# Optimization experiments

Measured on AMD Instinct MI355X. Metric: run time of the kernel, lower is better.

## Reference

```python
import jax, jax.numpy as jnp
import numpy as np

ALPHA = 0.2  # LeakyReLU negative slope
NEG = -9e15


def _gat_heads(x, adj_mask, W, a):
    # x: (B,N,F); W: (H,F,O); a: (H,2O); adj_mask: (B,N,N) bool
    O = W.shape[-1]
    Wh = jnp.einsum('bnf,hfo->bhno', x, W)            # (B,H,N,O)
    e1 = jnp.einsum('bhno,ho->bhn', Wh, a[:, :O])     # Wh @ a[:O]
    e2 = jnp.einsum('bhno,ho->bhn', Wh, a[:, O:])     # Wh @ a[O:]
    e = jax.nn.leaky_relu(e1[:, :, :, None] + e2[:, :, None, :], ALPHA)  # (B,H,N,N)
    e = jnp.where(adj_mask[:, None], e, NEG)
    attn = jax.nn.softmax(e, axis=-1)
    return jnp.einsum('bhnm,bhmo->bhno', attn, Wh)    # (B,H,N,O)


def _gat_block(x, adj_mask, non_pad_mask, W_heads, a_heads, W_out, a_out):
    # multi-head layer, concat=True -> elu per head, then concat on feature dim
    h = jax.nn.elu(_gat_heads(x, adj_mask, W_heads, a_heads))  # (B,H,N,O)
    B, H, N, O = h.shape
    h = jnp.transpose(h, (0, 2, 1, 3)).reshape(B, N, H * O)
    h = h * non_pad_mask
    # out layer: single head, concat=False (no inner elu)
    h = _gat_heads(h, adj_mask, W_out[None], a_out[None])[:, 0]  # (B,N,noutput)
    h = h * non_pad_mask
    return jax.nn.elu(h)


def setup_inputs() -> dict:
    key = jax.random.key(0)
    ks = jax.random.split(key, 8)
    B, N = 32, 256
    vocab, F, O, H, OUT = 200, 300, 256, 8, 512
    fea = jax.random.randint(ks[0], (B, N), 0, vocab, dtype=jnp.int32)
    adj = jax.random.randint(ks[1], (B, N, N), 0, 2, dtype=jnp.int32)
    non_pad_mask = jnp.ones((B, N, 1), dtype=jnp.float32)
    embed = jax.random.normal(ks[2], (vocab, F), dtype=jnp.float32)
    W_heads = jax.random.normal(ks[3], (H, F, O), dtype=jnp.float32) / np.sqrt(F)
    a_heads = jax.random.normal(ks[4], (H, 2 * O), dtype=jnp.float32) / np.sqrt(2 * O)
    W_out = jax.random.normal(ks[5], (H * O, OUT), dtype=jnp.float32) / np.sqrt(H * O)
    a_out = jax.random.normal(ks[6], (2 * OUT,), dtype=jnp.float32) / np.sqrt(2 * OUT)
    return {"fea": fea, "adj": adj, "non_pad_mask": non_pad_mask, "embed": embed,
            "W_heads": W_heads, "a_heads": a_heads, "W_out": W_out, "a_out": a_out}


def reference(fea, adj, non_pad_mask, embed, W_heads, a_heads, W_out, a_out):
    adj_mask = adj > 0
    x = embed[fea]  # (B,N,F)
    # GAT_num = 1; dropout is identity in eval mode
    x = _gat_block(x, adj_mask, non_pad_mask, W_heads, a_heads, W_out, a_out)
    return x  # (B, N, 512)
```

## Files before the change

kernel.cpp:

```cpp
#include <hip/hip_runtime.h>
#include <math.h>


typedef _Float16 f16;
typedef __attribute__((ext_vector_type(8))) _Float16 f16x8;
typedef __attribute__((ext_vector_type(4))) _Float16 f16x4;
typedef __attribute__((ext_vector_type(4))) float f32x4;

__device__ __forceinline__ void async16(const void* g, void* lds) {
  __builtin_amdgcn_global_load_lds(
      (const __attribute__((address_space(1))) void*)g,
      (__attribute__((address_space(3))) void*)lds, 16, 0, 0);
}

__global__ __launch_bounds__(256) void k_prep(const int* __restrict__ fea,
                                              const float* __restrict__ embed,
                                              const float* __restrict__ Whd,
                                              const float* __restrict__ Wo,
                                              f16* __restrict__ x16,
                                              f16* __restrict__ WcT,
                                              f16* __restrict__ WoT,
                                              float* __restrict__ e_all) {
  int bid = blockIdx.x, tid = threadIdx.x;
  if (bid < 1280) {
    int idx = bid * 256 + tid;
    int row = idx / 40, c = idx % 40;
    int tok = fea[row];
    const float* eb = embed + (size_t)tok * 300;
    f16x8 v;
#pragma unroll
    for (int j = 0; j < 8; ++j) {
      int t = c * 8 + j;
      v[j] = (f16)((t < 300) ? eb[t] : 0.f);
    }
    *(f16x8*)&x16[(size_t)row * 320 + c * 8] = v;
  } else if (bid < 1920) {
    int r = bid - 1280;
    int zi = r * 256 + tid;
    if (zi < 147456) e_all[zi] = 0.f;
    __shared__ float tile[32][33];
    int bx = r % 10, q0 = r / 10;
    int by = q0 % 8, h = q0 / 8;
    int c = tid & 31, q = tid >> 5;
#pragma unroll
    for (int i = 0; i < 4; ++i) {
      int tt = q + i * 8;
      int t = bx * 32 + tt;
      float v = (t < 300) ? Whd[((size_t)h * 300 + t) * 256 + by * 32 + c] : 0.f;
      tile[tt][c] = v;
    }
    __syncthreads();
#pragma unroll
    for (int i = 0; i < 4; ++i) {
      int oo = q + i * 8;
      int gc = h * 256 + by * 32 + oo;
      WcT[(size_t)gc * 320 + bx * 32 + c] = (f16)tile[c][oo];
    }
  } else {
    int r = bid - 1920;
    __shared__ float tile[32][33];
    int bx = r % 64, by = r / 64;
    int c = tid & 31, q = tid >> 5;
#pragma unroll
    for (int i = 0; i < 4; ++i) {
      int kk = q + i * 8;
      tile[kk][c] = Wo[((size_t)bx * 32 + kk) * 512 + by * 32 + c];
    }
    __syncthreads();
#pragma unroll
    for (int i = 0; i < 4; ++i) {
      int oo = q + i * 8;
      WoT[((size_t)by * 32 + oo) * 2048 + bx * 32 + c] = (f16)tile[c][oo];
    }
  }
}

template <int KDIM, int NCOLS>
__global__ __launch_bounds__(256, 4) void k_gemm1(const f16* __restrict__ A,
                                                  const f16* __restrict__ BT,
                                                  f16* __restrict__ outT,
                                                  const float* __restrict__ avec,
                                                  float* __restrict__ e1,
                                                  float* __restrict__ e2) {
  __shared__ f16 As[128 * 64];
  __shared__ f16 Bs[128 * 64];
  const int by = blockIdx.x, bx = blockIdx.y;
  const int tid = threadIdx.x;
  const int wave = tid >> 6, lane = tid & 63;
  const int wm = wave >> 1, wn = wave & 1;
  const int lrow = lane & 15, quad = lane >> 4;
  const int srow = lane >> 3;
  const int scol = ((lane & 7) ^ (lane >> 3)) * 8;
  const int l7 = lrow & 7;

  f32x4 acc[4][4] = {};
  const f16* Ag = A + (size_t)by * 128 * KDIM;
  const f16* Bg = BT + (size_t)bx * 128 * KDIM;

  for (int k0 = 0; k0 < KDIM; k0 += 64) {
    __syncthreads();
#pragma unroll
    for (int j = 0; j < 4; ++j) {
      const int r0 = wave * 32 + j * 8;
      async16(Ag + (size_t)(r0 + srow) * KDIM + k0 + scol, &As[r0 * 64]);
      async16(Bg + (size_t)(r0 + srow) * KDIM + k0 + scol, &Bs[r0 * 64]);
    }
    __syncthreads();
#pragma unroll
    for (int s = 0; s < 2; ++s) {
      const int sq = ((s * 4 + quad) ^ l7) * 8;
      f16x8 af[4], bf[4];
#pragma unroll
      for (int t = 0; t < 4; ++t) {
        af[t] = *(const f16x8*)&As[(wm * 64 + t * 16 + lrow) * 64 + sq];
        bf[t] = *(const f16x8*)&Bs[(wn * 64 + t * 16 + lrow) * 64 + sq];
      }
#pragma unroll
      for (int mt = 0; mt < 4; ++mt)
#pragma unroll
        for (int nt = 0; nt < 4; ++nt)
          acc[mt][nt] = __builtin_amdgcn_mfma_f32_16x16x32_f16(af[mt], bf[nt], acc[mt][nt], 0, 0, 0);
    }
  }

  const int b = (by * 128) >> 8;
  const int nbase0 = (by * 128) & 255;
#pragma unroll
  for (int mt = 0; mt < 4; ++mt) {
    const int nb = nbase0 + wm * 64 + mt * 16 + quad * 4;
#pragma unroll
    for (int nt = 0; nt < 4; ++nt) {
      const int gc = bx * 128 + wn * 64 + nt * 16 + lrow;
      f16x4 v;
#pragma unroll
      for (int r = 0; r < 4; ++r) v[r] = (f16)acc[mt][nt][r];
      *(f16x4*)&outT[((size_t)b * NCOLS + gc) * 256 + nb] = v;
    }
  }

  float a1v[4], a2v[4];
#pragma unroll
  for (int nt = 0; nt < 4; ++nt) {
    const int gc = bx * 128 + wn * 64 + nt * 16 + lrow;
    int hh = gc >> 8, oo = gc & 255;
    a1v[nt] = avec[hh * 512 + oo];
    a2v[nt] = avec[hh * 512 + 256 + oo];
  }
  const int hblk = (bx * 128) >> 8;
  const int ebase = (b * 8 + hblk) * 256;
#pragma unroll
  for (int mt = 0; mt < 4; ++mt) {
    float s1[4] = {0.f, 0.f, 0.f, 0.f}, s2[4] = {0.f, 0.f, 0.f, 0.f};
#pragma unroll
    for (int nt = 0; nt < 4; ++nt)
#pragma unroll
      for (int r = 0; r < 4; ++r) {
        s1[r] += acc[mt][nt][r] * a1v[nt];
        s2[r] += acc[mt][nt][r] * a2v[nt];
      }
#pragma unroll
    for (int r = 0; r < 4; ++r)
#pragma unroll
      for (int m = 1; m < 16; m <<= 1) {
        s1[r] += __shfl_xor(s1[r], m);
        s2[r] += __shfl_xor(s2[r], m);
      }
    if (lrow == 0) {
      const int nb = nbase0 + wm * 64 + mt * 16 + quad * 4;
#pragma unroll
      for (int r = 0; r < 4; ++r) {
        atomicAdd(&e1[ebase + nb + r], s1[r]);
        atomicAdd(&e2[ebase + nb + r], s2[r]);
      }
    }
  }
}

__global__ __launch_bounds__(256, 4) void k_gemm_sk(const f16* __restrict__ A,
                                                    const f16* __restrict__ BT,
                                                    f16* __restrict__ outSK) {
  __shared__ f16 As[128 * 64];
  __shared__ f16 Bs[64 * 64];
  const int by = blockIdx.x, bx = blockIdx.y, kz = blockIdx.z;
  const int tid = threadIdx.x;
  const int wave = tid >> 6, lane = tid & 63;
  const int wm = wave >> 1, wn = wave & 1;
  const int lrow = lane & 15, quad = lane >> 4;
  const int srow = lane >> 3;
  const int scol = ((lane & 7) ^ (lane >> 3)) * 8;
  const int l7 = lrow & 7;

  f32x4 acc[4][2] = {};
  const f16* Ag = A + (size_t)by * 128 * 2048;
  const f16* Bg = BT + (size_t)bx * 64 * 2048;
  const int kbeg = kz * 1024;

  for (int k0 = kbeg; k0 < kbeg + 1024; k0 += 64) {
    __syncthreads();
#pragma unroll
    for (int j = 0; j < 4; ++j) {
      const int r0 = wave * 32 + j * 8;
      async16(Ag + (size_t)(r0 + srow) * 2048 + k0 + scol, &As[r0 * 64]);
    }
#pragma unroll
    for (int j = 0; j < 2; ++j) {
      const int r0 = wave * 16 + j * 8;
      async16(Bg + (size_t)(r0 + srow) * 2048 + k0 + scol, &Bs[r0 * 64]);
    }
    __syncthreads();
#pragma unroll
    for (int s = 0; s < 2; ++s) {
      const int sq = ((s * 4 + quad) ^ l7) * 8;
      f16x8 af[4], bf[2];
#pragma unroll
      for (int t = 0; t < 4; ++t)
        af[t] = *(const f16x8*)&As[(wm * 64 + t * 16 + lrow) * 64 + sq];
#pragma unroll
      for (int t = 0; t < 2; ++t)
        bf[t] = *(const f16x8*)&Bs[(wn * 32 + t * 16 + lrow) * 64 + sq];
#pragma unroll
      for (int mt = 0; mt < 4; ++mt)
#pragma unroll
        for (int nt = 0; nt < 2; ++nt)
          acc[mt][nt] = __builtin_amdgcn_mfma_f32_16x16x32_f16(af[mt], bf[nt], acc[mt][nt], 0, 0, 0);
    }
  }

  const int b = (by * 128) >> 8;
  const int nbase0 = (by * 128) & 255;
  f16* dst = outSK + (size_t)kz * 32 * 512 * 256;
#pragma unroll
  for (int mt = 0; mt < 4; ++mt) {
    const int nb = nbase0 + wm * 64 + mt * 16 + quad * 4;
#pragma unroll
    for (int nt = 0; nt < 2; ++nt) {
      const int gc = bx * 64 + wn * 32 + nt * 16 + lrow;
      f16x4 v;
#pragma unroll
      for (int r = 0; r < 4; ++r) v[r] = (f16)acc[mt][nt][r];
      *(f16x4*)&dst[((size_t)b * 512 + gc) * 256 + nb] = v;
    }
  }
}

__global__ void k_comb(const f16* __restrict__ sk, const float* __restrict__ ao,
                       f16* __restrict__ Wh2T, float* __restrict__ e12,
                       float* __restrict__ e22) {
  int oc = blockIdx.x;
  int b = blockIdx.y;
  int n = threadIdx.x;
  const f16* b0 = sk + ((size_t)b * 512 + oc * 32) * 256 + n;
  const f16* b1 = b0 + (size_t)32 * 512 * 256;
  f16* wbase = Wh2T + ((size_t)b * 512 + oc * 32) * 256 + n;
  float s1 = 0.f, s2 = 0.f;
#pragma unroll 8
  for (int j = 0; j < 32; ++j) {
    float v = (float)b0[(size_t)j * 256] + (float)b1[(size_t)j * 256];
    int o2 = oc * 32 + j;
    s1 += v * ao[o2];
    s2 += v * ao[512 + o2];
    wbase[(size_t)j * 256] = (f16)v;
  }
  atomicAdd(&e12[b * 256 + n], s1);
  atomicAdd(&e22[b * 256 + n], s2);
}

#define PSTRIDE 264

__global__ __launch_bounds__(256, 4) void k_attn1(
    const f16* __restrict__ WhT, const float* __restrict__ e1g, const float* __restrict__ e2g,
    const int* __restrict__ adj, const float* __restrict__ npm, f16* __restrict__ h1) {
  int h = blockIdx.x, b = blockIdx.y, nt0 = blockIdx.z;
  int bh = b * 8 + h;
  int n0 = nt0 * 64;
  __shared__ f16 P[64 * PSTRIDE];
  int tid = threadIdx.x;
  int wave = tid >> 6, lane = tid & 63;

  float4 e2v = *(const float4*)&e2g[bh * 256 + lane * 4];
  float e2m = fmaxf(fmaxf(e2v.x, e2v.y), fmaxf(e2v.z, e2v.w));
#pragma unroll
  for (int m = 1; m < 64; m <<= 1) e2m = fmaxf(e2m, __shfl_xor(e2m, m));
#pragma unroll 4
  for (int i = 0; i < 16; ++i) {
    int row = i * 4 + wave;
    int gn = b * 256 + n0 + row;
    float er = e1g[bh * 256 + n0 + row];
    float sh = er + e2m;
    sh = sh > 0.f ? sh : 0.2f * sh;
    int4 aj = *(const int4*)&adj[(size_t)gn * 256 + lane * 4];
    float p0, p1, p2, p3;
    {
      float v = er + e2v.x; v = v > 0.f ? v : 0.2f * v;
      p0 = aj.x ? __expf(v - sh) : 0.f;
      v = er + e2v.y; v = v > 0.f ? v : 0.2f * v;
      p1 = aj.y ? __expf(v - sh) : 0.f;
      v = er + e2v.z; v = v > 0.f ? v : 0.2f * v;
      p2 = aj.z ? __expf(v - sh) : 0.f;
      v = er + e2v.w; v = v > 0.f ? v : 0.2f * v;
      p3 = aj.w ? __expf(v - sh) : 0.f;
    }
    float sm = p0 + p1 + p2 + p3;
#pragma unroll
    for (int m = 1; m < 64; m <<= 1) sm += __shfl_xor(sm, m);
    float rs = 1.f / sm;
    f16x4 pw;
    pw[0] = (f16)(p0 * rs); pw[1] = (f16)(p1 * rs);
    pw[2] = (f16)(p2 * rs); pw[3] = (f16)(p3 * rs);
    *(f16x4*)&P[row * PSTRIDE + lane * 4] = pw;
  }
  __syncthreads();

  int lrow = lane & 15, quad = lane >> 4;
  f32x4 acc[4][4] = {};
  const f16* Ag = WhT + (size_t)bh * 65536;
#pragma unroll 2
  for (int k0 = 0; k0 < 256; k0 += 32) {
    f16x8 af[4], bf[4];
#pragma unroll
    for (int mt = 0; mt < 4; ++mt)
      af[mt] = *(const f16x8*)&Ag[(size_t)(wave * 64 + mt * 16 + lrow) * 256 + k0 + quad * 8];
#pragma unroll
    for (int nt = 0; nt < 4; ++nt)
      bf[nt] = *(const f16x8*)&P[(nt * 16 + lrow) * PSTRIDE + k0 + quad * 8];
#pragma unroll
    for (int mt = 0; mt < 4; ++mt)
#pragma unroll
      for (int nt = 0; nt < 4; ++nt)
        acc[mt][nt] = __builtin_amdgcn_mfma_f32_16x16x32_f16(af[mt], bf[nt], acc[mt][nt], 0, 0, 0);
  }
#pragma unroll
  for (int nt = 0; nt < 4; ++nt) {
    int nloc = nt * 16 + lrow;
    int gn = b * 256 + n0 + nloc;
    float pm = npm[gn];
#pragma unroll
    for (int mt = 0; mt < 4; ++mt) {
      int o0 = wave * 64 + mt * 16 + quad * 4;
      f16x4 st;
#pragma unroll
      for (int r = 0; r < 4; ++r) {
        float v = acc[mt][nt][r];
        v = v > 0.f ? v : (__expf(v) - 1.f);
        st[r] = (f16)(v * pm);
      }
      *(f16x4*)&h1[(size_t)gn * 2048 + h * 256 + o0] = st;
    }
  }
}

__global__ __launch_bounds__(256, 4) void k_attn2(
    const f16* __restrict__ Wh2T, const float* __restrict__ e1g, const float* __restrict__ e2g,
    const int* __restrict__ adj, const float* __restrict__ npm, float* __restrict__ out) {
  int oh = blockIdx.x, b = blockIdx.y, nt0 = blockIdx.z;
  int n0 = nt0 * 64;
  __shared__ f16 P[64 * PSTRIDE];
  int tid = threadIdx.x;
  int wave = tid >> 6, lane = tid & 63;

  float4 e2v = *(const float4*)&e2g[b * 256 + lane * 4];
  float e2m = fmaxf(fmaxf(e2v.x, e2v.y), fmaxf(e2v.z, e2v.w));
#pragma unroll
  for (int m = 1; m < 64; m <<= 1) e2m = fmaxf(e2m, __shfl_xor(e2m, m));
#pragma unroll 4
  for (int i = 0; i < 16; ++i) {
    int row = i * 4 + wave;
    int gn = b * 256 + n0 + row;
    float er = e1g[b * 256 + n0 + row];
    float sh = er + e2m;
    sh = sh > 0.f ? sh : 0.2f * sh;
    int4 aj = *(const int4*)&adj[(size_t)gn * 256 + lane * 4];
    float p0, p1, p2, p3;
    {
      float v = er + e2v.x; v = v > 0.f ? v : 0.2f * v;
      p0 = aj.x ? __expf(v - sh) : 0.f;
      v = er + e2v.y; v = v > 0.f ? v : 0.2f * v;
      p1 = aj.y ? __expf(v - sh) : 0.f;
      v = er + e2v.z; v = v > 0.f ? v : 0.2f * v;
      p2 = aj.z ? __expf(v - sh) : 0.f;
      v = er + e2v.w; v = v > 0.f ? v : 0.2f * v;
      p3 = aj.w ? __expf(v - sh) : 0.f;
    }
    float sm = p0 + p1 + p2 + p3;
#pragma unroll
    for (int m = 1; m < 64; m <<= 1) sm += __shfl_xor(sm, m);
    float rs = 1.f / sm;
    f16x4 pw;
    pw[0] = (f16)(p0 * rs); pw[1] = (f16)(p1 * rs);
    pw[2] = (f16)(p2 * rs); pw[3] = (f16)(p3 * rs);
    *(f16x4*)&P[row * PSTRIDE + lane * 4] = pw;
  }
  __syncthreads();

  int lrow = lane & 15, quad = lane >> 4;
  f32x4 acc[4][4] = {};
  const f16* Ag = Wh2T + (size_t)b * 512 * 256 + (size_t)oh * 65536;
#pragma unroll 2
  for (int k0 = 0; k0 < 256; k0 += 32) {
    f16x8 af[4], bf[4];
#pragma unroll
    for (int mt = 0; mt < 4; ++mt)
      af[mt] = *(const f16x8*)&Ag[(size_t)(wave * 64 + mt * 16 + lrow) * 256 + k0 + quad * 8];
#pragma unroll
    for (int nt = 0; nt < 4; ++nt)
      bf[nt] = *(const f16x8*)&P[(nt * 16 + lrow) * PSTRIDE + k0 + quad * 8];
#pragma unroll
    for (int mt = 0; mt < 4; ++mt)
#pragma unroll
      for (int nt = 0; nt < 4; ++nt)
        acc[mt][nt] = __builtin_amdgcn_mfma_f32_16x16x32_f16(af[mt], bf[nt], acc[mt][nt], 0, 0, 0);
  }
#pragma unroll
  for (int nt = 0; nt < 4; ++nt) {
    int nloc = nt * 16 + lrow;
    int gn = b * 256 + n0 + nloc;
    float pm = npm[gn];
#pragma unroll
    for (int mt = 0; mt < 4; ++mt) {
      int o0 = oh * 256 + wave * 64 + mt * 16 + quad * 4;
      float4 st;
      float v0 = acc[mt][nt][0] * pm;
      float v1 = acc[mt][nt][1] * pm;
      float v2 = acc[mt][nt][2] * pm;
      float v3 = acc[mt][nt][3] * pm;
      st.x = v0 > 0.f ? v0 : (__expf(v0) - 1.f);
      st.y = v1 > 0.f ? v1 : (__expf(v1) - 1.f);
      st.z = v2 > 0.f ? v2 : (__expf(v2) - 1.f);
      st.w = v3 > 0.f ? v3 : (__expf(v3) - 1.f);
      *(float4*)&out[(size_t)gn * 512 + o0] = st;
    }
  }
}

extern "C" void kernel_launch(void* const* d_in, const int* in_sizes, int n_in,
                              void* d_out, int out_size, void* d_ws, size_t ws_size,
                              hipStream_t stream) {
  (void)in_sizes; (void)n_in; (void)out_size; (void)ws_size;
  const int*   fea   = (const int*)d_in[0];
  const int*   adj   = (const int*)d_in[1];
  const float* npm   = (const float*)d_in[2];
  const float* embed = (const float*)d_in[3];
  const float* Whd   = (const float*)d_in[4];
  const float* ah    = (const float*)d_in[5];
  const float* Wo    = (const float*)d_in[6];
  const float* ao    = (const float*)d_in[7];
  float* out = (float*)d_out;

  char* ws = (char*)d_ws;
  f16* x16  = (f16*)ws;  ws += (size_t)8192 * 320 * 2;
  f16* WcT  = (f16*)ws;  ws += (size_t)2048 * 320 * 2;
  f16* WoT  = (f16*)ws;  ws += (size_t)512 * 2048 * 2;
  f16* WhT  = (f16*)ws;  ws += (size_t)32 * 8 * 256 * 256 * 2;
  f16* h1   = (f16*)ws;  ws += (size_t)8192 * 2048 * 2;
  f16* Wh2T = (f16*)ws;  ws += (size_t)32 * 512 * 256 * 2;
  f16* Wh2sk = (f16*)ws; ws += (size_t)2 * 32 * 512 * 256 * 2;
  float* e1  = (float*)ws; ws += (size_t)65536 * 4;
  float* e2  = (float*)ws; ws += (size_t)65536 * 4;
  float* e12 = (float*)ws; ws += (size_t)8192 * 4;
  float* e22 = (float*)ws; ws += (size_t)8192 * 4;

  k_prep<<<2944, 256, 0, stream>>>(fea, embed, Whd, Wo, x16, WcT, WoT, e1);

  k_gemm1<320, 2048><<<dim3(64, 16), 256, 0, stream>>>(x16, WcT, WhT, ah, e1, e2);
  k_attn1<<<dim3(8, 32, 4), 256, 0, stream>>>(WhT, e1, e2, adj, npm, h1);

  k_gemm_sk<<<dim3(64, 8, 2), 256, 0, stream>>>(h1, WoT, Wh2sk);
  k_comb<<<dim3(16, 32), 256, 0, stream>>>(Wh2sk, ao, Wh2T, e12, e22);
  k_attn2<<<dim3(2, 32, 4), 256, 0, stream>>>(Wh2T, e12, e22, adj, npm, out);
}
```

Measured before the change: 204.9 us.

## Fold split-K combine into GEMM epilogue and attention operand load

Removes the k_comb kernel. The split-K GEMM epilogue now computes the e12/e22 projections directly via shuffle reductions and atomics. k_attn2 sums the two split-K partial halves on the fly while loading its A operand. k_attn2 is regridded to 4 column chunks of 128 with half the accumulators, which saves a launch and an intermediate write/read but doubles the global reads of the A operand inside attention. The summed f16 values differ slightly in rounding, since the partials are added in f16 instead of f32.

```diff
diff --git a/kernel.cpp b/kernel.cpp
--- a/kernel.cpp
+++ b/kernel.cpp
@@ -178,7 +178,10 @@
 
 __global__ __launch_bounds__(256, 4) void k_gemm_sk(const f16* __restrict__ A,
                                                     const f16* __restrict__ BT,
-                                                    f16* __restrict__ outSK) {
+                                                    f16* __restrict__ outSK,
+                                                    const float* __restrict__ ao,
+                                                    float* __restrict__ e12,
+                                                    float* __restrict__ e22) {
   __shared__ f16 As[128 * 64];
   __shared__ f16 Bs[64 * 64];
   const int by = blockIdx.x, bx = blockIdx.y, kz = blockIdx.z;
@@ -241,28 +244,40 @@
       *(f16x4*)&dst[((size_t)b * 512 + gc) * 256 + nb] = v;
     }
   }
-}
-
-__global__ void k_comb(const f16* __restrict__ sk, const float* __restrict__ ao,
-                       f16* __restrict__ Wh2T, float* __restrict__ e12,
-                       float* __restrict__ e22) {
-  int oc = blockIdx.x;
-  int b = blockIdx.y;
-  int n = threadIdx.x;
-  const f16* b0 = sk + ((size_t)b * 512 + oc * 32) * 256 + n;
-  const f16* b1 = b0 + (size_t)32 * 512 * 256;
-  f16* wbase = Wh2T + ((size_t)b * 512 + oc * 32) * 256 + n;
-  float s1 = 0.f, s2 = 0.f;
-#pragma unroll 8
-  for (int j = 0; j < 32; ++j) {
-    float v = (float)b0[(size_t)j * 256] + (float)b1[(size_t)j * 256];
-    int o2 = oc * 32 + j;
-    s1 += v * ao[o2];
-    s2 += v * ao[512 + o2];
-    wbase[(size_t)j * 256] = (f16)v;
-  }
-  atomicAdd(&e12[b * 256 + n], s1);
-  atomicAdd(&e22[b * 256 + n], s2);
+
+  float a1v[2], a2v[2];
+#pragma unroll
+  for (int nt = 0; nt < 2; ++nt) {
+    const int gc = bx * 64 + wn * 32 + nt * 16 + lrow;
+    a1v[nt] = ao[gc];
+    a2v[nt] = ao[512 + gc];
+  }
+#pragma unroll
+  for (int mt = 0; mt < 4; ++mt) {
+    float s1[4] = {0.f, 0.f, 0.f, 0.f}, s2[4] = {0.f, 0.f, 0.f, 0.f};
+#pragma unroll
+    for (int nt = 0; nt < 2; ++nt)
+#pragma unroll
+      for (int r = 0; r < 4; ++r) {
+        s1[r] += acc[mt][nt][r] * a1v[nt];
+        s2[r] += acc[mt][nt][r] * a2v[nt];
+      }
+#pragma unroll
+    for (int r = 0; r < 4; ++r)
+#pragma unroll
+      for (int m = 1; m < 16; m <<= 1) {
+        s1[r] += __shfl_xor(s1[r], m);
+        s2[r] += __shfl_xor(s2[r], m);
+      }
+    if (lrow == 0) {
+      const int nb = nbase0 + wm * 64 + mt * 16 + quad * 4;
+#pragma unroll
+      for (int r = 0; r < 4; ++r) {
+        atomicAdd(&e12[b * 256 + nb + r], s1[r]);
+        atomicAdd(&e22[b * 256 + nb + r], s2[r]);
+      }
+    }
+  }
 }
 
 #define PSTRIDE 264
@@ -350,7 +365,7 @@
 }
 
 __global__ __launch_bounds__(256, 4) void k_attn2(
-    const f16* __restrict__ Wh2T, const float* __restrict__ e1g, const float* __restrict__ e2g,
+    const f16* __restrict__ sk, const float* __restrict__ e1g, const float* __restrict__ e2g,
     const int* __restrict__ adj, const float* __restrict__ npm, float* __restrict__ out) {
   int oh = blockIdx.x, b = blockIdx.y, nt0 = blockIdx.z;
   int n0 = nt0 * 64;
@@ -393,19 +408,22 @@
   __syncthreads();
 
   int lrow = lane & 15, quad = lane >> 4;
-  f32x4 acc[4][4] = {};
-  const f16* Ag = Wh2T + (size_t)b * 512 * 256 + (size_t)oh * 65536;
+  f32x4 acc[2][4] = {};
+  const f16* Ag0 = sk + ((size_t)b * 512 + oh * 128) * 256;
+  const f16* Ag1 = Ag0 + (size_t)32 * 512 * 256;
 #pragma unroll 2
   for (int k0 = 0; k0 < 256; k0 += 32) {
-    f16x8 af[4], bf[4];
-#pragma unroll
-    for (int mt = 0; mt < 4; ++mt)
-      af[mt] = *(const f16x8*)&Ag[(size_t)(wave * 64 + mt * 16 + lrow) * 256 + k0 + quad * 8];
+    f16x8 af[2], bf[4];
+#pragma unroll
+    for (int mt = 0; mt < 2; ++mt) {
+      size_t off = (size_t)(wave * 32 + mt * 16 + lrow) * 256 + k0 + quad * 8;
+      af[mt] = *(const f16x8*)&Ag0[off] + *(const f16x8*)&Ag1[off];
+    }
 #pragma unroll
     for (int nt = 0; nt < 4; ++nt)
       bf[nt] = *(const f16x8*)&P[(nt * 16 + lrow) * PSTRIDE + k0 + quad * 8];
 #pragma unroll
-    for (int mt = 0; mt < 4; ++mt)
+    for (int mt = 0; mt < 2; ++mt)
 #pragma unroll
       for (int nt = 0; nt < 4; ++nt)
         acc[mt][nt] = __builtin_amdgcn_mfma_f32_16x16x32_f16(af[mt], bf[nt], acc[mt][nt], 0, 0, 0);
@@ -416,8 +434,8 @@
     int gn = b * 256 + n0 + nloc;
     float pm = npm[gn];
 #pragma unroll
-    for (int mt = 0; mt < 4; ++mt) {
-      int o0 = oh * 256 + wave * 64 + mt * 16 + quad * 4;
+    for (int mt = 0; mt < 2; ++mt) {
+      int o0 = oh * 128 + wave * 32 + mt * 16 + quad * 4;
       float4 st;
       float v0 = acc[mt][nt][0] * pm;
       float v1 = acc[mt][nt][1] * pm;
@@ -452,7 +470,6 @@
   f16* WoT  = (f16*)ws;  ws += (size_t)512 * 2048 * 2;
   f16* WhT  = (f16*)ws;  ws += (size_t)32 * 8 * 256 * 256 * 2;
   f16* h1   = (f16*)ws;  ws += (size_t)8192 * 2048 * 2;
-  f16* Wh2T = (f16*)ws;  ws += (size_t)32 * 512 * 256 * 2;
   f16* Wh2sk = (f16*)ws; ws += (size_t)2 * 32 * 512 * 256 * 2;
   float* e1  = (float*)ws; ws += (size_t)65536 * 4;
   float* e2  = (float*)ws; ws += (size_t)65536 * 4;
@@ -464,7 +481,6 @@
   k_gemm1<320, 2048><<<dim3(64, 16), 256, 0, stream>>>(x16, WcT, WhT, ah, e1, e2);
   k_attn1<<<dim3(8, 32, 4), 256, 0, stream>>>(WhT, e1, e2, adj, npm, h1);
 
-  k_gemm_sk<<<dim3(64, 8, 2), 256, 0, stream>>>(h1, WoT, Wh2sk);
-  k_comb<<<dim3(16, 32), 256, 0, stream>>>(Wh2sk, ao, Wh2T, e12, e22);
-  k_attn2<<<dim3(2, 32, 4), 256, 0, stream>>>(Wh2T, e12, e22, adj, npm, out);
-}
+  k_gemm_sk<<<dim3(64, 8, 2), 256, 0, stream>>>(h1, WoT, Wh2sk, ao, e12, e22);
+  k_attn2<<<dim3(4, 32, 4), 256, 0, stream>>>(Wh2sk, e12, e22, adj, npm, out);
+}
```

Result: no change. 201.9 us (-1.4%).
